# Performance work log

Measured on AMD Instinct MI355X. Metric: run time of the kernel, lower is better.

## Reference

```python
import jax, jax.numpy as jnp
import numpy as np

NH, NP = 8, 4  # n_heads, n_points
SHAPES = [(100, 167), (50, 84), (25, 42), (13, 21)]  # (H, W) per level


def setup_inputs() -> dict:
    key = jax.random.key(0)
    ks = jax.random.split(key, 8)
    bs, dm = 2, 256
    nl = len(SHAPES)
    nv = sum(h * w for h, w in SHAPES)  # 22223
    nq = nv
    s = 1.0 / np.sqrt(dm)
    return {
        'query': jax.random.normal(ks[0], (bs, nq, dm), jnp.float32),
        'value': jax.random.normal(ks[1], (bs, nv, dm), jnp.float32),
        'reference_points': jax.random.uniform(ks[2], (bs, nq, nl, 2), jnp.float32),
        'W_so': jax.random.normal(ks[3], (dm, NH * nl * NP * 2), jnp.float32) * 0.01,
        'b_so': jax.random.normal(ks[4], (NH * nl * NP * 2,), jnp.float32) * 0.5,
        'W_aw': jax.random.normal(ks[5], (dm, NH * nl * NP), jnp.float32) * s,
        'b_aw': jnp.zeros((NH * nl * NP,), jnp.float32),
        'W_vp': jax.random.normal(ks[6], (dm, dm), jnp.float32) * s,
        'b_vp': jnp.zeros((dm,), jnp.float32),
        'W_op': jax.random.normal(ks[7], (dm, dm), jnp.float32) * s,
        'b_op': jnp.zeros((dm,), jnp.float32),
        'spatial_shapes': jnp.array(SHAPES, jnp.int32),
    }


def _bilinear_gather(vf, H, W, loc):
    # vf: [BH, H*W, dh] flattened level feature map; loc: [BH, QP, 2] in [0,1]
    # Matches torch grid_sample(mode='bilinear', padding_mode='zeros', align_corners=False)
    x = loc[..., 0] * W - 0.5
    y = loc[..., 1] * H - 0.5
    x0f = jnp.floor(x); y0f = jnp.floor(y)
    lx = x - x0f; ly = y - y0f
    x0 = x0f.astype(jnp.int32); y0 = y0f.astype(jnp.int32)
    out = jnp.zeros(vf.shape[:1] + loc.shape[1:2] + vf.shape[-1:], vf.dtype)
    for dx, dy, w in ((0, 0, (1 - lx) * (1 - ly)), (1, 0, lx * (1 - ly)),
                      (0, 1, (1 - lx) * ly), (1, 1, lx * ly)):
        xi = x0 + dx; yi = y0 + dy
        valid = (xi >= 0) & (xi < W) & (yi >= 0) & (yi < H)
        idx = jnp.clip(yi, 0, H - 1) * W + jnp.clip(xi, 0, W - 1)  # [BH, QP]
        g = jnp.take_along_axis(vf, idx[:, :, None], axis=1)  # [BH, QP, dh]
        out = out + g * (w * valid)[:, :, None]
    return out


def _msda(value_heads, shapes_np, loc, aw):
    # value_heads: [bs,nv,nh,dh], loc: [bs,nq,nh,nl,np,2], aw: [bs,nq,nh,nl,np]
    bs, nv, nh, dh = value_heads.shape
    nq, nl, npnt = loc.shape[1], loc.shape[3], loc.shape[4]
    out = jnp.zeros((bs * nh, nq, dh), value_heads.dtype)
    start = 0
    for lvl in range(nl):
        H, W = int(shapes_np[lvl, 0]), int(shapes_np[lvl, 1])
        vf = value_heads[:, start:start + H * W].transpose(0, 2, 1, 3).reshape(bs * nh, H * W, dh)
        loc_l = loc[:, :, :, lvl].transpose(0, 2, 1, 3, 4).reshape(bs * nh, nq * npnt, 2)
        samp = _bilinear_gather(vf, H, W, loc_l).reshape(bs * nh, nq, npnt, dh)
        aw_l = aw[:, :, :, lvl].transpose(0, 2, 1, 3).reshape(bs * nh, nq, npnt)
        out = out + jnp.einsum('bqpd,bqp->bqd', samp, aw_l)
        start += H * W
    return out.reshape(bs, nh, nq, dh).transpose(0, 2, 1, 3).reshape(bs, nq, nh * dh)


def reference(query, value, reference_points, W_so, b_so, W_aw, b_aw, W_vp, b_vp, W_op, b_op, spatial_shapes):
    bs, nq, dm = query.shape
    nl = reference_points.shape[2]
    dh = dm // NH
    v = (value @ W_vp + b_vp).reshape(bs, value.shape[1], NH, dh)
    off = (query @ W_so + b_so).reshape(bs, nq, NH, nl, NP, 2)
    aw = jax.nn.softmax((query @ W_aw + b_aw).reshape(bs, nq, NH, nl * NP), axis=-1)
    aw = aw.reshape(bs, nq, NH, nl, NP)
    ss = np.asarray(spatial_shapes)  # static level metadata
    normalizer = jnp.asarray(np.stack([ss[:, 1], ss[:, 0]], -1), query.dtype)  # (w, h) per level
    loc = reference_points[:, :, None, :, None, :] + off / normalizer[None, None, None, :, None, :]
    out = _msda(v, ss, loc, aw)
    return out @ W_op + b_op + query  # identity residual (identity defaults to query)
```

## Files before the change

### kernel.cpp

```cpp
#include <hip/hip_runtime.h>
#include <hip/hip_bf16.h>
#include <math.h>

typedef __hip_bfloat16 bf16;
using f32x4  = __attribute__((ext_vector_type(4))) float;
using f32x2  = __attribute__((ext_vector_type(2))) float;
using bf16x8 = __attribute__((ext_vector_type(8))) short;
using f16x2  = __attribute__((ext_vector_type(2))) _Float16;

constexpr int BS = 2, NQ = 22223, MROWS = 44446;
constexpr int LH[4] = {100, 50, 25, 13};
constexpr int LW[4] = {167, 84, 42, 21};
constexpr int LSTART[4] = {0, 16700, 20900, 21950};
constexpr int PLW[4] = {170, 87, 45, 24};
constexpr int PLSTART[4] = {0, 17510, 22121, 23381};
constexpr int PTOT = 23765;

constexpr int BM = 128, BK = 32;
constexpr int LDT = 40;
constexpr int GX = (MROWS + BM - 1) / BM;

__global__ __launch_bounds__(256) void prep_weights(
    const float* __restrict__ W_vp, const float* __restrict__ W_so,
    const float* __restrict__ W_aw, const float* __restrict__ W_op,
    const float* __restrict__ b_so, const float* __restrict__ b_aw,
    bf16* __restrict__ Wt_vp, bf16* __restrict__ Wt_cat,
    bf16* __restrict__ Wt_op, float* __restrict__ bcat)
{
    int i = blockIdx.x * 256 + threadIdx.x;
    if (i < 256 * 256) {
        int n = i >> 8, k = i & 255;
        Wt_vp[i] = __float2bfloat16(W_vp[k * 256 + n]);
        Wt_op[i] = __float2bfloat16(W_op[k * 256 + n]);
    }
    if (i < 384 * 256) {
        int n = i >> 8, k = i & 255;
        float v = (n < 256) ? W_so[k * 256 + n] : W_aw[k * 128 + (n - 256)];
        Wt_cat[i] = __float2bfloat16(v);
    }
    if (i < 384) bcat[i] = (i < 256) ? b_so[i] : b_aw[i - 256];
}

__device__ inline int pad_base_idx(int pix) {
    if (pix < LSTART[1])      { int y = pix / 167;                  int x = pix - y * 167;                return PLSTART[0] + (y + 1) * 170 + (x + 1); }
    else if (pix < LSTART[2]) { int rel = pix - LSTART[1]; int y = rel / 84; int x = rel - y * 84;        return PLSTART[1] + (y + 1) * 87  + (x + 1); }
    else if (pix < LSTART[3]) { int rel = pix - LSTART[2]; int y = rel / 42; int x = rel - y * 42;        return PLSTART[2] + (y + 1) * 45  + (x + 1); }
    else                      { int rel = pix - LSTART[3]; int y = rel / 21; int x = rel - y * 21;        return PLSTART[3] + (y + 1) * 24  + (x + 1); }
}

template<bool A_BF16>
__device__ __forceinline__ void mfma_core(
    const void* __restrict__ Av, int lda, const bf16* __restrict__ Wt,
    int row0, int bn0, int M, bf16* As, bf16* Bs, f32x4 (&acc)[4][4])
{
    const int tid = threadIdx.x;
    const int lane = tid & 63;
    const int wv = tid >> 6;
    const int wm = (wv >> 1) * 64, wn = (wv & 1) * 64;
    const int l15 = lane & 15, l4 = lane >> 4;

#pragma unroll
    for (int m = 0; m < 4; ++m)
#pragma unroll
        for (int n = 0; n < 4; ++n) { acc[m][n][0]=0.f; acc[m][n][1]=0.f; acc[m][n][2]=0.f; acc[m][n][3]=0.f; }

    for (int k0 = 0; k0 < 256; k0 += BK) {
        __syncthreads();
#pragma unroll
        for (int t = 0; t < 2; ++t) {
            int idx = tid + t * 256;
            int r = idx >> 2, s = idx & 3;
            {
                int grow = row0 + r; if (grow >= M) grow = M - 1;
                bf16 tmp[8];
                if constexpr (A_BF16) {
                    const bf16* ap = (const bf16*)Av + (size_t)grow * lda + (k0 + s * 8);
                    *(uint4*)tmp = *(const uint4*)ap;
                } else {
                    const float* ap = (const float*)Av + (size_t)grow * lda + (k0 + s * 8);
                    f32x4 v0 = *(const f32x4*)ap;
                    f32x4 v1 = *(const f32x4*)(ap + 4);
#pragma unroll
                    for (int j = 0; j < 4; ++j) tmp[j] = __float2bfloat16(v0[j]);
#pragma unroll
                    for (int j = 0; j < 4; ++j) tmp[4 + j] = __float2bfloat16(v1[j]);
                }
                *(uint4*)&As[r * LDT + s * 8] = *(const uint4*)tmp;
            }
            *(uint4*)&Bs[r * LDT + s * 8] =
                *(const uint4*)(Wt + (size_t)(bn0 + r) * 256 + (k0 + s * 8));
        }
        __syncthreads();

        bf16x8 af[4], bfr[4];
#pragma unroll
        for (int m = 0; m < 4; ++m)
            af[m] = *(const bf16x8*)&As[(wm + m * 16 + l15) * LDT + l4 * 8];
#pragma unroll
        for (int n = 0; n < 4; ++n)
            bfr[n] = *(const bf16x8*)&Bs[(wn + n * 16 + l15) * LDT + l4 * 8];
#pragma unroll
        for (int m = 0; m < 4; ++m)
#pragma unroll
            for (int n = 0; n < 4; ++n)
                acc[m][n] = __builtin_amdgcn_mfma_f32_16x16x32_bf16(af[m], bfr[n], acc[m][n], 0, 0, 0);
    }
}

__global__ __launch_bounds__(256) void gemm_producer(
    const float* __restrict__ query, const float* __restrict__ value,
    const bf16* __restrict__ Wt_cat, const bf16* __restrict__ Wt_vp,
    const float* __restrict__ bcat, const float* __restrict__ bvp,
    bf16* __restrict__ offawl, _Float16* __restrict__ vproj)
{
    __shared__ bf16 As[BM * LDT];
    __shared__ bf16 Bs[BM * LDT];

    constexpr int NWG = GX * 5;
    constexpr int QXW = NWG / 8, RXW = NWG % 8;
    int orig = blockIdx.x;
    int xcd = orig & 7, seq = orig >> 3;
    int swz = (xcd < RXW ? xcd * (QXW + 1) : RXW * (QXW + 1) + (xcd - RXW) * QXW) + seq;
    int slice = swz % 5;
    int row0 = (swz / 5) * BM;

    const bool isOff = slice < 3;
    const void* A = isOff ? (const void*)query : (const void*)value;
    const bf16* Wt = isOff ? Wt_cat : Wt_vp;
    const float* bias = isOff ? bcat : bvp;
    int bn0 = isOff ? slice * 128 : (slice - 3) * 128;

    f32x4 acc[4][4];
    mfma_core<false>(A, 256, Wt, row0, bn0, MROWS, As, Bs, acc);

    const int lane = threadIdx.x & 63;
    const int wv = threadIdx.x >> 6;
    const int wm = (wv >> 1) * 64, wn = (wv & 1) * 64;
    const int l15 = lane & 15, l4 = lane >> 4;

    if (isOff) {
#pragma unroll
        for (int m = 0; m < 4; ++m)
#pragma unroll
            for (int j = 0; j < 4; ++j) {
                int r = row0 + wm + m * 16 + l4 * 4 + j;
                if (r < MROWS) {
                    bf16* orow = offawl + (size_t)r * 384;
#pragma unroll
                    for (int n = 0; n < 4; ++n) {
                        int fcol = bn0 + wn + n * 16 + l15;
                        orow[fcol] = __float2bfloat16(acc[m][n][j] + bias[fcol]);
                    }
                }
            }
    } else {
#pragma unroll
        for (int m = 0; m < 4; ++m)
#pragma unroll
            for (int j = 0; j < 4; ++j) {
                int r = row0 + wm + m * 16 + l4 * 4 + j;
                if (r < MROWS) {
                    int bb = (r >= NQ) ? 1 : 0;
                    int pb = pad_base_idx(r - bb * NQ);
#pragma unroll
                    for (int n = 0; n < 4; ++n) {
                        int fcol = bn0 + wn + n * 16 + l15;
                        int hh = fcol >> 5, cc = fcol & 31;
                        vproj[((size_t)(hh * 2 + bb) * PTOT + pb) * 32 + cc] =
                            (_Float16)(acc[m][n][j] + bias[fcol]);
                    }
                }
            }
    }
}

__global__ __launch_bounds__(256) void gemm_out(
    const bf16* __restrict__ msda, const bf16* __restrict__ Wt_op,
    const float* __restrict__ b_op, const float* __restrict__ query,
    float* __restrict__ out)
{
    __shared__ bf16 As[BM * LDT];
    __shared__ bf16 Bs[BM * LDT];

    constexpr int NWG = GX * 2;
    int orig = blockIdx.x;
    int swz = (orig & 7) * (NWG / 8) + (orig >> 3);
    int bn0 = (swz & 1) * 128;
    int row0 = (swz >> 1) * BM;

    f32x4 acc[4][4];
    mfma_core<true>(msda, 384, Wt_op, row0, bn0, MROWS, As, Bs, acc);

    const int lane = threadIdx.x & 63;
    const int wv = threadIdx.x >> 6;
    const int wm = (wv >> 1) * 64, wn = (wv & 1) * 64;
    const int l15 = lane & 15, l4 = lane >> 4;

#pragma unroll
    for (int m = 0; m < 4; ++m)
#pragma unroll
        for (int j = 0; j < 4; ++j) {
            int r = row0 + wm + m * 16 + l4 * 4 + j;
            if (r < MROWS) {
#pragma unroll
                for (int n = 0; n < 4; ++n) {
                    int fcol = bn0 + wn + n * 16 + l15;
                    out[(size_t)r * 256 + fcol] =
                        acc[m][n][j] + b_op[fcol] + query[(size_t)r * 256 + fcol];
                }
            }
        }
}

__device__ inline f32x2 bfpair(unsigned u) {
    f32x2 r;
    r.x = __uint_as_float(u << 16);
    r.y = __uint_as_float(u & 0xffff0000u);
    return r;
}

__global__ __launch_bounds__(256)
__attribute__((amdgpu_waves_per_eu(2, 4)))
void msda_sample10(
    const _Float16* __restrict__ vproj,
    const bf16* __restrict__ offawl,
    const float* __restrict__ refp,
    bf16* __restrict__ msda_out)
{
    __shared__ uint2 sOA[8][128];
    __shared__ float sRef[8][8];

    constexpr int NBLK = (MROWS + 7) / 8;
    constexpr int QX = NBLK / 8, RX = NBLK % 8;
    const int orig = blockIdx.x;
    const int xcd = orig & 7, seq = orig >> 3;
    const int blk = (xcd < RX ? xcd * (QX + 1) : RX * (QX + 1) + (xcd - RX) * QX) + seq;
    const int q0 = blk * 8;

    const int tid = threadIdx.x;

#pragma unroll
    for (int k = 0; k < 4; ++k) {
        int idx = tid + k * 256;
        int row = idx >> 7, e = idx & 127;
        if (e < 96) {
            int grow = min(q0 + row, MROWS - 1);
            sOA[row][e] = *((const uint2*)(offawl + (size_t)grow * 384) + e);
        }
    }
    if (tid < 64) {
        int row = tid >> 3, er = tid & 7;
        int grow = min(q0 + row, MROWS - 1);
        sRef[row][er] = refp[(size_t)grow * 8 + er];
    }
    __syncthreads();

    const int w = tid >> 6;
    const int lane = tid & 63;
    const int qs = lane >> 5;
    const int h = (lane >> 2) & 7;
    const int s = lane & 3;
    const int qrow = w * 2 + qs;
    int q = q0 + qrow;
    const bool alive = q < MROWS;
    if (!alive) q = MROWS - 1;
    const int b = (q >= NQ) ? 1 : 0;

    const char* rowp = (const char*)&sOA[qrow][0];
    unsigned off16[16];
    {
        uint4 o0 = *(const uint4*)(rowp + h * 64);
        uint4 o1 = *(const uint4*)(rowp + h * 64 + 16);
        uint4 o2 = *(const uint4*)(rowp + h * 64 + 32);
        uint4 o3 = *(const uint4*)(rowp + h * 64 + 48);
        off16[0]=o0.x; off16[1]=o0.y; off16[2]=o0.z; off16[3]=o0.w;
        off16[4]=o1.x; off16[5]=o1.y; off16[6]=o1.z; off16[7]=o1.w;
        off16[8]=o2.x; off16[9]=o2.y; off16[10]=o2.z; off16[11]=o2.w;
        off16[12]=o3.x; off16[13]=o3.y; off16[14]=o3.z; off16[15]=o3.w;
    }

    float aw[16];
    {
        uint4 g0 = *(const uint4*)(rowp + 512 + h * 32);
        uint4 g1 = *(const uint4*)(rowp + 512 + h * 32 + 16);
        unsigned gu[8] = {g0.x,g0.y,g0.z,g0.w,g1.x,g1.y,g1.z,g1.w};
        float lg[16];
#pragma unroll
        for (int i = 0; i < 8; ++i) {
            f32x2 p = bfpair(gu[i]);
            lg[2*i] = p.x; lg[2*i+1] = p.y;
        }
        float mx = lg[0];
#pragma unroll
        for (int i = 1; i < 16; ++i) mx = fmaxf(mx, lg[i]);
        float ssum = 0.f;
#pragma unroll
        for (int i = 0; i < 16; ++i) { aw[i] = __expf(lg[i] - mx); ssum += aw[i]; }
        float inv = 1.f / ssum;
#pragma unroll
        for (int i = 0; i < 16; ++i) aw[i] *= inv;
    }

    f16x2 acc0 = {0, 0}, acc1 = {0, 0}, acc2 = {0, 0}, acc3 = {0, 0};

#pragma unroll
    for (int l = 0; l < 4; ++l) {
        const int W = LW[l], H = LH[l], Wp = PLW[l];
        const float xb = sRef[qrow][l * 2 + 0] * (float)W + 0.5f;
        const float yb = sRef[qrow][l * 2 + 1] * (float)H + 0.5f;
        const _Float16* vl = vproj + ((size_t)(h * 2 + b) * PTOT + PLSTART[l]) * 32 + s * 8;

        const _Float16* pp[4];
        f16x2 hw[4][4];
#pragma unroll
        for (int p = 0; p < 4; ++p) {
            const int t = l * 4 + p;
            f32x2 o2 = bfpair(off16[t]);
            float x = fminf(fmaxf(xb + o2.x, 0.f), (float)(W + 1));
            float y = fminf(fmaxf(yb + o2.y, 0.f), (float)(H + 1));
            float x0f = floorf(x), y0f = floorf(y);
            float lx = x - x0f, ly = y - y0f;
            int x0 = (int)x0f, y0 = (int)y0f;
            pp[p] = vl + (size_t)((y0 * Wp + x0) * 32);
            float aww = aw[t];
            float wx0 = 1.f - lx;
            float wy0 = (1.f - ly) * aww, wy1 = ly * aww;
            _Float16 h00 = (_Float16)(wx0 * wy0), h01 = (_Float16)(lx * wy0);
            _Float16 h10 = (_Float16)(wx0 * wy1), h11 = (_Float16)(lx * wy1);
            hw[p][0] = f16x2{h00, h00}; hw[p][1] = f16x2{h01, h01};
            hw[p][2] = f16x2{h10, h10}; hw[p][3] = f16x2{h11, h11};
        }

        uint4 c[4][4];
#pragma unroll
        for (int p = 0; p < 4; ++p) {
            c[p][0] = *(const uint4*)(pp[p]);
            c[p][1] = *(const uint4*)(pp[p] + 32);
            c[p][2] = *(const uint4*)(pp[p] + Wp * 32);
            c[p][3] = *(const uint4*)(pp[p] + Wp * 32 + 32);
        }

#pragma unroll
        for (int p = 0; p < 4; ++p)
#pragma unroll
            for (int cc = 0; cc < 4; ++cc) {
                acc0 += __builtin_bit_cast(f16x2, c[p][cc].x) * hw[p][cc];
                acc1 += __builtin_bit_cast(f16x2, c[p][cc].y) * hw[p][cc];
                acc2 += __builtin_bit_cast(f16x2, c[p][cc].z) * hw[p][cc];
                acc3 += __builtin_bit_cast(f16x2, c[p][cc].w) * hw[p][cc];
            }
    }

    if (alive) {
        bf16 ob[8];
        ob[0] = __float2bfloat16((float)acc0[0]);
        ob[1] = __float2bfloat16((float)acc0[1]);
        ob[2] = __float2bfloat16((float)acc1[0]);
        ob[3] = __float2bfloat16((float)acc1[1]);
        ob[4] = __float2bfloat16((float)acc2[0]);
        ob[5] = __float2bfloat16((float)acc2[1]);
        ob[6] = __float2bfloat16((float)acc3[0]);
        ob[7] = __float2bfloat16((float)acc3[1]);
        *(uint4*)(msda_out + (size_t)q * 384 + h * 32 + s * 8) = *(const uint4*)ob;
    }
}

extern "C" void kernel_launch(void* const* d_in, const int* in_sizes, int n_in,
                              void* d_out, int out_size, void* d_ws, size_t ws_size,
                              hipStream_t stream) {
    const float* query = (const float*)d_in[0];
    const float* value = (const float*)d_in[1];
    const float* refp  = (const float*)d_in[2];
    const float* W_so  = (const float*)d_in[3];
    const float* b_so  = (const float*)d_in[4];
    const float* W_aw  = (const float*)d_in[5];
    const float* b_aw  = (const float*)d_in[6];
    const float* W_vp  = (const float*)d_in[7];
    const float* b_vp  = (const float*)d_in[8];
    const float* W_op  = (const float*)d_in[9];
    const float* b_op  = (const float*)d_in[10];
    float* out = (float*)d_out;

    bf16*     d_offawl = (bf16*)d_ws;
    _Float16* d_vproj  = (_Float16*)(d_offawl + (size_t)MROWS * 384);
    bf16*     d_wtcat  = (bf16*)(d_vproj + (size_t)16 * PTOT * 32);
    bf16*     d_wtvp   = d_wtcat + 384 * 256;
    bf16*     d_wtop   = d_wtvp + 256 * 256;
    float*    d_bcat   = (float*)(d_wtop + 256 * 256);

    prep_weights<<<384, 256, 0, stream>>>(W_vp, W_so, W_aw, W_op, b_so, b_aw,
                                          d_wtvp, d_wtcat, d_wtop, d_bcat);
    hipMemsetAsync(d_vproj, 0, (size_t)16 * PTOT * 32 * sizeof(_Float16), stream);

    gemm_producer<<<GX * 5, 256, 0, stream>>>(
        query, value, d_wtcat, d_wtvp, d_bcat, b_vp, d_offawl, d_vproj);

    msda_sample10<<<(MROWS + 7) / 8, 256, 0, stream>>>(
        d_vproj, d_offawl, refp, d_offawl);

    gemm_out<<<GX * 2, 256, 0, stream>>>(d_offawl, d_wtop, b_op, query, out);
}
```

Measured before the change: 164.3 us.

## Split bilinear corners across lane pairs in MSDA sampling with shuffle reduction

The sampling kernel now gives each wave one query instead of two, with 8 lanes per head. The lanes are split into two groups that each fetch one x-column of the bilinear corners, and the partial sums are combined with an xor shuffle. Blocks now cover 4 queries, so the grid doubles and per-thread gathers halve, which exposes more memory-level parallelism for the latency-bound gather. In exchange it uses twice as many threads, adds a cross-lane reduction with extra fp16 rounding, and duplicates the offset and softmax math across lanes.

Result: faster. 153.0 us (-6.9%).

```diff
diff --git a/kernel.cpp b/kernel.cpp
--- a/kernel.cpp
+++ b/kernel.cpp
@@ -221,34 +221,32 @@
 
 __global__ __launch_bounds__(256)
 __attribute__((amdgpu_waves_per_eu(2, 4)))
-void msda_sample10(
+void msda_sample14(
     const _Float16* __restrict__ vproj,
     const bf16* __restrict__ offawl,
     const float* __restrict__ refp,
     bf16* __restrict__ msda_out)
 {
-    __shared__ uint2 sOA[8][128];
-    __shared__ float sRef[8][8];
-
-    constexpr int NBLK = (MROWS + 7) / 8;
-    constexpr int QX = NBLK / 8, RX = NBLK % 8;
+    __shared__ uint2 sOA[4][96];
+    __shared__ float sRef[4][8];
+
+    constexpr int NBLK = (MROWS + 3) / 4;
     const int orig = blockIdx.x;
-    const int xcd = orig & 7, seq = orig >> 3;
-    const int blk = (xcd < RX ? xcd * (QX + 1) : RX * (QX + 1) + (xcd - RX) * QX) + seq;
-    const int q0 = blk * 8;
+    const int blk = (orig & 7) * (NBLK / 8) + (orig >> 3);
+    const int q0 = blk * 4;
 
     const int tid = threadIdx.x;
 
 #pragma unroll
-    for (int k = 0; k < 4; ++k) {
+    for (int k = 0; k < 2; ++k) {
         int idx = tid + k * 256;
-        int row = idx >> 7, e = idx & 127;
-        if (e < 96) {
+        if (idx < 384) {
+            int row = idx / 96, e = idx - (idx / 96) * 96;
             int grow = min(q0 + row, MROWS - 1);
             sOA[row][e] = *((const uint2*)(offawl + (size_t)grow * 384) + e);
         }
     }
-    if (tid < 64) {
+    if (tid < 32) {
         int row = tid >> 3, er = tid & 7;
         int grow = min(q0 + row, MROWS - 1);
         sRef[row][er] = refp[(size_t)grow * 8 + er];
@@ -257,27 +255,16 @@
 
     const int w = tid >> 6;
     const int lane = tid & 63;
-    const int qs = lane >> 5;
-    const int h = (lane >> 2) & 7;
-    const int s = lane & 3;
-    const int qrow = w * 2 + qs;
-    int q = q0 + qrow;
+    const int h = lane >> 3;
+    const int s = lane & 7;
+    const int sx = s >> 2;
+    const int c16 = s & 3;
+    int q = q0 + w;
     const bool alive = q < MROWS;
     if (!alive) q = MROWS - 1;
     const int b = (q >= NQ) ? 1 : 0;
 
-    const char* rowp = (const char*)&sOA[qrow][0];
-    unsigned off16[16];
-    {
-        uint4 o0 = *(const uint4*)(rowp + h * 64);
-        uint4 o1 = *(const uint4*)(rowp + h * 64 + 16);
-        uint4 o2 = *(const uint4*)(rowp + h * 64 + 32);
-        uint4 o3 = *(const uint4*)(rowp + h * 64 + 48);
-        off16[0]=o0.x; off16[1]=o0.y; off16[2]=o0.z; off16[3]=o0.w;
-        off16[4]=o1.x; off16[5]=o1.y; off16[6]=o1.z; off16[7]=o1.w;
-        off16[8]=o2.x; off16[9]=o2.y; off16[10]=o2.z; off16[11]=o2.w;
-        off16[12]=o3.x; off16[13]=o3.y; off16[14]=o3.z; off16[15]=o3.w;
-    }
+    const char* rowp = (const char*)&sOA[w][0];
 
     float aw[16];
     {
@@ -306,52 +293,61 @@
 #pragma unroll
     for (int l = 0; l < 4; ++l) {
         const int W = LW[l], H = LH[l], Wp = PLW[l];
-        const float xb = sRef[qrow][l * 2 + 0] * (float)W + 0.5f;
-        const float yb = sRef[qrow][l * 2 + 1] * (float)H + 0.5f;
-        const _Float16* vl = vproj + ((size_t)(h * 2 + b) * PTOT + PLSTART[l]) * 32 + s * 8;
-
-        const _Float16* pp[4];
-        f16x2 hw[4][4];
+        const float xb = sRef[w][l * 2 + 0] * (float)W + 0.5f;
+        const float yb = sRef[w][l * 2 + 1] * (float)H + 0.5f;
+        const _Float16* vl = vproj + ((size_t)(h * 2 + b) * PTOT + PLSTART[l]) * 32 + c16 * 8;
+
+        const _Float16* pr[4][2];
+        f16x2 hwv[4][2];
 #pragma unroll
         for (int p = 0; p < 4; ++p) {
-            const int t = l * 4 + p;
-            f32x2 o2 = bfpair(off16[t]);
+            unsigned ov = *(const unsigned*)(rowp + h * 64 + (l * 4 + p) * 4);
+            f32x2 o2 = bfpair(ov);
             float x = fminf(fmaxf(xb + o2.x, 0.f), (float)(W + 1));
             float y = fminf(fmaxf(yb + o2.y, 0.f), (float)(H + 1));
             float x0f = floorf(x), y0f = floorf(y);
             float lx = x - x0f, ly = y - y0f;
             int x0 = (int)x0f, y0 = (int)y0f;
-            pp[p] = vl + (size_t)((y0 * Wp + x0) * 32);
-            float aww = aw[t];
-            float wx0 = 1.f - lx;
-            float wy0 = (1.f - ly) * aww, wy1 = ly * aww;
-            _Float16 h00 = (_Float16)(wx0 * wy0), h01 = (_Float16)(lx * wy0);
-            _Float16 h10 = (_Float16)(wx0 * wy1), h11 = (_Float16)(lx * wy1);
-            hw[p][0] = f16x2{h00, h00}; hw[p][1] = f16x2{h01, h01};
-            hw[p][2] = f16x2{h10, h10}; hw[p][3] = f16x2{h11, h11};
-        }
-
-        uint4 c[4][4];
+            pr[p][0] = vl + (size_t)((y0 * Wp + x0 + sx) * 32);
+            pr[p][1] = pr[p][0] + Wp * 32;
+            float wxs = sx ? lx : (1.f - lx);
+            float a = aw[l * 4 + p];
+            _Float16 e0 = (_Float16)(wxs * (1.f - ly) * a);
+            _Float16 e1 = (_Float16)(wxs * ly * a);
+            hwv[p][0] = f16x2{e0, e0};
+            hwv[p][1] = f16x2{e1, e1};
+        }
+
+        uint4 c[4][2];
 #pragma unroll
         for (int p = 0; p < 4; ++p) {
-            c[p][0] = *(const uint4*)(pp[p]);
-            c[p][1] = *(const uint4*)(pp[p] + 32);
-            c[p][2] = *(const uint4*)(pp[p] + Wp * 32);
-            c[p][3] = *(const uint4*)(pp[p] + Wp * 32 + 32);
+            c[p][0] = *(const uint4*)pr[p][0];
+            c[p][1] = *(const uint4*)pr[p][1];
         }
 
 #pragma unroll
         for (int p = 0; p < 4; ++p)
 #pragma unroll
-            for (int cc = 0; cc < 4; ++cc) {
-                acc0 += __builtin_bit_cast(f16x2, c[p][cc].x) * hw[p][cc];
-                acc1 += __builtin_bit_cast(f16x2, c[p][cc].y) * hw[p][cc];
-                acc2 += __builtin_bit_cast(f16x2, c[p][cc].z) * hw[p][cc];
-                acc3 += __builtin_bit_cast(f16x2, c[p][cc].w) * hw[p][cc];
-            }
-    }
-
-    if (alive) {
+            for (int r = 0; r < 2; ++r) {
+                acc0 += __builtin_bit_cast(f16x2, c[p][r].x) * hwv[p][r];
+                acc1 += __builtin_bit_cast(f16x2, c[p][r].y) * hwv[p][r];
+                acc2 += __builtin_bit_cast(f16x2, c[p][r].z) * hwv[p][r];
+                acc3 += __builtin_bit_cast(f16x2, c[p][r].w) * hwv[p][r];
+            }
+    }
+
+    {
+        unsigned u0 = __builtin_bit_cast(unsigned, acc0);
+        unsigned u1 = __builtin_bit_cast(unsigned, acc1);
+        unsigned u2 = __builtin_bit_cast(unsigned, acc2);
+        unsigned u3 = __builtin_bit_cast(unsigned, acc3);
+        acc0 += __builtin_bit_cast(f16x2, __shfl_xor((int)u0, 4));
+        acc1 += __builtin_bit_cast(f16x2, __shfl_xor((int)u1, 4));
+        acc2 += __builtin_bit_cast(f16x2, __shfl_xor((int)u2, 4));
+        acc3 += __builtin_bit_cast(f16x2, __shfl_xor((int)u3, 4));
+    }
+
+    if (alive && sx == 0) {
         bf16 ob[8];
         ob[0] = __float2bfloat16((float)acc0[0]);
         ob[1] = __float2bfloat16((float)acc0[1]);
@@ -361,7 +357,7 @@
         ob[5] = __float2bfloat16((float)acc2[1]);
         ob[6] = __float2bfloat16((float)acc3[0]);
         ob[7] = __float2bfloat16((float)acc3[1]);
-        *(uint4*)(msda_out + (size_t)q * 384 + h * 32 + s * 8) = *(const uint4*)ob;
+        *(uint4*)(msda_out + (size_t)q * 384 + h * 32 + c16 * 8) = *(const uint4*)ob;
     }
 }
 
@@ -395,7 +391,7 @@
     gemm_producer<<<GX * 5, 256, 0, stream>>>(
         query, value, d_wtcat, d_wtvp, d_bcat, b_vp, d_offawl, d_vproj);
 
-    msda_sample10<<<(MROWS + 7) / 8, 256, 0, stream>>>(
+    msda_sample14<<<(MROWS + 3) / 4, 256, 0, stream>>>(
         d_vproj, d_offawl, refp, d_offawl);
 
     gemm_out<<<GX * 2, 256, 0, stream>>>(d_offawl, d_wtop, b_op, query, out);
```
